# Kernel optimization log

Measured on AMD Instinct MI355X. Metric: run time of the kernel, lower is better.

## Reference

```python
import jax, jax.numpy as jnp
import numpy as np

N = 20000; E = 320000; G = 64; IN = 64; HID = 128; H = 8; HD = H * HID  # 1024


def setup_inputs() -> dict:
    key = jax.random.key(0)
    ks = jax.random.split(key, 32)
    inp = {}
    inp['x'] = jax.random.normal(ks[0], (N, IN), jnp.float32)
    inp['edge_index'] = jax.random.randint(ks[1], (2, E), 0, N, dtype=jnp.int64)
    inp['batch'] = jnp.sort(jax.random.randint(ks[2], (N,), 0, G, dtype=jnp.int64))
    dims_in = [IN, HD, HD]
    k = 3
    for i in range(3):
        d_in = dims_in[i]
        inp[f'gat_W{i}'] = jax.random.normal(ks[k], (d_in, HD), jnp.float32) * (1.0 / np.sqrt(d_in)); k += 1
        inp[f'gat_b{i}'] = jnp.zeros((HD,), jnp.float32)
        inp[f'att_src{i}'] = jax.random.normal(ks[k], (H, HID), jnp.float32) * 0.1; k += 1
        inp[f'att_dst{i}'] = jax.random.normal(ks[k], (H, HID), jnp.float32) * 0.1; k += 1
    for i in range(2):
        inp[f'boot_W{i}'] = jax.random.normal(ks[k], (HD, HD), jnp.float32) * (1.0 / np.sqrt(HD)); k += 1
        inp[f'boot_b{i}'] = jnp.zeros((HD,), jnp.float32)
    inp['clf_W1'] = jax.random.normal(ks[k], (HD, HID), jnp.float32) * (1.0 / np.sqrt(HD)); k += 1
    inp['clf_b1'] = jnp.zeros((HID,), jnp.float32)
    inp['clf_W2'] = jax.random.normal(ks[k], (HID, 2), jnp.float32) * (1.0 / np.sqrt(HID)); k += 1
    inp['clf_b2'] = jnp.zeros((2,), jnp.float32)
    return inp


def _gat_layer(x, W, b, a_src, a_dst, src, dst):
    # PyG GATConv (concat=True, self-loops already appended, eval mode => no dropout)
    h = (x @ W).reshape(N, H, HID)                      # [N,H,D]
    s = jnp.einsum('nhd,hd->nh', h, a_src)              # [N,H]
    t = jnp.einsum('nhd,hd->nh', h, a_dst)              # [N,H]
    e = jax.nn.leaky_relu(s[src] + t[dst], 0.2)         # [Etot,H]
    m = jax.ops.segment_max(e, dst, num_segments=N)     # segment softmax over incoming edges
    m = jnp.where(jnp.isfinite(m), m, 0.0)
    ex = jnp.exp(e - m[dst])
    denom = jax.ops.segment_sum(ex, dst, num_segments=N)
    alpha = ex / jnp.maximum(denom[dst], 1e-16)         # [Etot,H]
    out = jax.ops.segment_sum(alpha[:, :, None] * h[src], dst, num_segments=N)  # [N,H,D]
    return out.reshape(N, HD) + b


def reference(x, edge_index, batch,
              gat_W0, gat_b0, att_src0, att_dst0,
              gat_W1, gat_b1, att_src1, att_dst1,
              gat_W2, gat_b2, att_src2, att_dst2,
              boot_W0, boot_b0, boot_W1, boot_b1,
              clf_W1, clf_b1, clf_W2, clf_b2):
    loop = jnp.arange(N, dtype=edge_index.dtype)
    src = jnp.concatenate([edge_index[0], loop])
    dst = jnp.concatenate([edge_index[1], loop])
    gat = [(gat_W0, gat_b0, att_src0, att_dst0),
           (gat_W1, gat_b1, att_src1, att_dst1),
           (gat_W2, gat_b2, att_src2, att_dst2)]
    boot = [(boot_W0, boot_b0), (boot_W1, boot_b1)]
    h = x
    for i in range(3):
        W, b, a_s, a_d = gat[i]
        h = jax.nn.elu(_gat_layer(h, W, b, a_s, a_d, src, dst))
        if i < 2:
            noise = jax.random.normal(jax.random.key(100 + i), h.shape, h.dtype) * 0.1
            bW, bb = boot[i]
            h = (h + noise) @ bW + bb
    # global mean pool over graphs
    sums = jax.ops.segment_sum(h, batch, num_segments=G)        # [G,HD]
    cnts = jax.ops.segment_sum(jnp.ones((N,), h.dtype), batch, num_segments=G)
    g = sums / jnp.maximum(cnts, 1.0)[:, None]
    z = jax.nn.relu(g @ clf_W1 + clf_b1)                        # dropout = identity (eval)
    return z @ clf_W2 + clf_b2
```

## Files before the change

### kernel.cpp

```cpp
#include <hip/hip_runtime.h>
#include <stdint.h>

#define N_NODES 20000
#define N_EDGES 320000
#define E_TOT   (N_EDGES + N_NODES)
#define NGRAPH  64
#define DIN     64
#define DHID    128
#define NHEAD   8
#define HDIM    1024

typedef unsigned int u32;
typedef unsigned short u16;
typedef __bf16 bfx8 __attribute__((ext_vector_type(8)));
typedef float f32x4 __attribute__((ext_vector_type(4)));
typedef float f32x2 __attribute__((ext_vector_type(2)));

__device__ __forceinline__ u16 f2bf(float f){
  u32 u = __float_as_uint(f);
  u32 r = (u + 0x7FFFu + ((u >> 16) & 1u)) >> 16;
  return (u16)r;
}
__device__ __forceinline__ float bf2f(u16 v){
  return __uint_as_float(((u32)v) << 16);
}

typedef __attribute__((address_space(3))) u32 lds_u32_t;
typedef const __attribute__((address_space(1))) u32 glb_u32_t;
__device__ __forceinline__ void g2l16(const void* g, void* l){
  __builtin_amdgcn_global_load_lds((glb_u32_t*)(uintptr_t)g,
                                   (lds_u32_t*)(uintptr_t)l, 16, 0, 0);
}

__device__ __forceinline__ u32 rotl32(u32 x, int r){ return (x<<r) | (x>>(32-r)); }

__device__ __forceinline__ void threefry2x32(u32 k0, u32 k1, u32 x0, u32 x1,
                                             u32& y0, u32& y1){
  u32 k2 = k0 ^ k1 ^ 0x1BD11BDAu;
  x0 += k0; x1 += k1;
#define TFR(r) { x0 += x1; x1 = rotl32(x1, (r)); x1 ^= x0; }
  TFR(13) TFR(15) TFR(26) TFR(6)
  x0 += k1; x1 += k2 + 1u;
  TFR(17) TFR(29) TFR(16) TFR(24)
  x0 += k2; x1 += k0 + 2u;
  TFR(13) TFR(15) TFR(26) TFR(6)
  x0 += k0; x1 += k1 + 3u;
  TFR(17) TFR(29) TFR(16) TFR(24)
  x0 += k1; x1 += k2 + 4u;
  TFR(13) TFR(15) TFR(26) TFR(6)
  x0 += k2; x1 += k0 + 5u;
#undef TFR
  y0 = x0; y1 = x1;
}

__device__ __forceinline__ float erfinv_fast(float x){
  float t = fmaf(-x, x, 1.0f);
  float w = -__logf(t);
  float p;
  if (w < 5.0f){
    w -= 2.5f;
    p = 2.81022636e-08f;
    p = fmaf(p, w, 3.43273939e-07f);
    p = fmaf(p, w, -3.5233877e-06f);
    p = fmaf(p, w, -4.39150654e-06f);
    p = fmaf(p, w, 0.00021858087f);
    p = fmaf(p, w, -0.00125372503f);
    p = fmaf(p, w, -0.00417768164f);
    p = fmaf(p, w, 0.246640727f);
    p = fmaf(p, w, 1.50140941f);
  } else {
    w = sqrtf(w) - 3.0f;
    p = -0.000200214257f;
    p = fmaf(p, w, 0.000100950558f);
    p = fmaf(p, w, 0.00134934322f);
    p = fmaf(p, w, -0.00367342844f);
    p = fmaf(p, w, 0.00573950773f);
    p = fmaf(p, w, -0.0076224613f);
    p = fmaf(p, w, 0.00943887047f);
    p = fmaf(p, w, 1.00167406f);
    p = fmaf(p, w, 2.83297682f);
  }
  return p * x;
}

__device__ __forceinline__ float jax_normal(u32 seed, u32 i){
  u32 y0, y1;
  threefry2x32(0u, seed, 0u, i, y0, y1);
  u32 bits = y0 ^ y1;
  float f = __uint_as_float((bits >> 9) | 0x3f800000u) - 1.0f;
  float xx = fmaxf(-0.99999994f, fmaf(f, 2.0f, -0.99999994f));
  return 1.41421356f * erfinv_fast(xx);
}

__global__ __launch_bounds__(256) void convert3_kernel(const float* __restrict__ x,
    const float* __restrict__ W0, const float* __restrict__ W1,
    u16* __restrict__ xbf, u16* __restrict__ O0, u16* __restrict__ O1){
  const int z = blockIdx.y;
  const float* S = (z==0) ? W0 : (z==1) ? W1 : x;
  u16* D = (z==0) ? O0 : (z==1) ? O1 : xbf;
  const int total = (z==2) ? N_NODES*DIN : HDIM*HDIM;
  int i = (blockIdx.x*256 + threadIdx.x)*4;
  if (i < total){
    float4 v = *(const float4*)(S + i);
    D[i+0] = f2bf(v.x); D[i+1] = f2bf(v.y);
    D[i+2] = f2bf(v.z); D[i+3] = f2bf(v.w);
  }
}

__global__ __launch_bounds__(256) void transpose_all_kernel(
    const float* __restrict__ W0, const float* __restrict__ W1,
    const float* __restrict__ W2, const float* __restrict__ W3,
    const float* __restrict__ W4,
    u16* __restrict__ T0, u16* __restrict__ T1, u16* __restrict__ T2,
    u16* __restrict__ T3, u16* __restrict__ T4){
  const int z = blockIdx.z;
  const float* W = (z==0)?W0:(z==1)?W1:(z==2)?W2:(z==3)?W3:W4;
  u16* T = (z==0)?T0:(z==1)?T1:(z==2)?T2:(z==3)?T3:T4;
  const int K = (z==0)?DIN:HDIM;
  const int bk = blockIdx.y*32;
  if (bk >= K) return;
  __shared__ float t[32][33];
  int bn = blockIdx.x*32;
  int lx = threadIdx.x & 31, ly = threadIdx.x >> 5;
#pragma unroll
  for (int r = 0; r < 32; r += 8)
    t[ly+r][lx] = W[(size_t)(bk+ly+r)*HDIM + bn + lx];
  __syncthreads();
#pragma unroll
  for (int r = 0; r < 32; r += 8)
    T[(size_t)(bn+ly+r)*K + bk + lx] = f2bf(t[lx][ly+r]);
}

__global__ __launch_bounds__(256) void bias_pair_kernel(
    const float* __restrict__ bb0, const u16* __restrict__ gwt0,
    const float* __restrict__ bb1, const u16* __restrict__ gwt1,
    float* __restrict__ out0, float* __restrict__ out1){
  const float* bb = blockIdx.y ? bb1 : bb0;
  const u16* gwt  = blockIdx.y ? gwt1 : gwt0;
  float* out      = blockIdx.y ? out1 : out0;
  const int wv = threadIdx.x >> 6, lane = threadIdx.x & 63;
  const int n = blockIdx.x*4 + wv;
  const u16* row = gwt + (size_t)n*HDIM + lane*16;
  const float* bp = bb + lane*16;
  float acc = 0.f;
#pragma unroll
  for (int k = 0; k < 16; ++k) acc = fmaf(bp[k], bf2f(row[k]), acc);
  for (int off = 32; off > 0; off >>= 1) acc += __shfl_down(acc, off);
  if (lane == 0) out[n] = acc;
}

__global__ __launch_bounds__(256) void count_all_kernel(const int* __restrict__ ei,
    const int* __restrict__ batch, int* __restrict__ cnt, int* __restrict__ gcnt){
  int i = blockIdx.x*256 + threadIdx.x;
  if (i < N_EDGES) atomicAdd(&cnt[ei[N_EDGES + i]], 1);
  else if (i < N_EDGES + N_NODES) atomicAdd(&gcnt[batch[i - N_EDGES]], 1);
}

__global__ __launch_bounds__(1024) void scan_rowptr_kernel(const int* __restrict__ cnt,
    int* __restrict__ rowptr, int* __restrict__ cursor){
  __shared__ int wsum[16];
  __shared__ int carry_s;
  const int tid = threadIdx.x, lane = tid & 63, wv = tid >> 6;
  if (tid == 0){ carry_s = 0; rowptr[0] = 0; }
  __syncthreads();
  for (int base = 0; base < N_NODES; base += 1024){
    int i = base + tid;
    int v = (i < N_NODES) ? cnt[i] + 1 : 0;
    int s = v;
#pragma unroll
    for (int off = 1; off < 64; off <<= 1){
      int t = __shfl_up(s, off);
      if (lane >= off) s += t;
    }
    if (lane == 63) wsum[wv] = s;
    __syncthreads();
    if (wv == 0 && lane < 16){
      int ws = wsum[lane];
#pragma unroll
      for (int off = 1; off < 16; off <<= 1){
        int t = __shfl_up(ws, off);
        if (lane >= off) ws += t;
      }
      wsum[lane] = ws;
    }
    __syncthreads();
    int incl = s + ((wv > 0) ? wsum[wv-1] : 0) + carry_s;
    if (i < N_NODES){ rowptr[i+1] = incl; cursor[i] = incl - v; }
    __syncthreads();
    if (tid == 1023) carry_s = incl;
    __syncthreads();
  }
}

__global__ __launch_bounds__(256) void fill_self_kernel(int* __restrict__ cursor,
    int* __restrict__ colidx){
  int n = blockIdx.x*256 + threadIdx.x;
  if (n < N_NODES){ int p = atomicAdd(&cursor[n], 1); colidx[p] = n; }
}

__global__ __launch_bounds__(256) void fill_edges_kernel(const int* __restrict__ ei,
    int* __restrict__ cursor, int* __restrict__ colidx){
  int e = blockIdx.x*256 + threadIdx.x;
  if (e < N_EDGES){
    int s = ei[e], d = ei[N_EDGES + e];
    int p = atomicAdd(&cursor[d], 1);
    colidx[p] = s;
  }
}

__global__ void scan_gcnt_kernel(const int* __restrict__ gcnt, int* __restrict__ goff){
  if (threadIdx.x == 0){
    int s = 0;
    for (int g = 0; g < NGRAPH; ++g){ goff[g] = s; s += gcnt[g]; }
    goff[NGRAPH] = s;
  }
}

__device__ __forceinline__ void gemm_tile(const u16* __restrict__ A,
    const u16* __restrict__ BT, const float* __restrict__ bias,
    u16* __restrict__ Cb, int M, int K, int bm, int bn,
    u16* As, u16* Bs){
  const int tid = threadIdx.x;
  const int lane = tid & 63, w = tid >> 6;
  const int wm = (w & 1)*64, wn = (w >> 1)*64;

  const int cid0 = tid, cid1 = 256 + tid;
  const int r0 = cid0 & 127, kc0 = cid0 >> 7;
  const int r1 = cid1 & 127, kc1 = cid1 >> 7;
  int ar0 = bm + r0; if (ar0 >= M) ar0 = M - 1;
  int ar1 = bm + r1; if (ar1 >= M) ar1 = M - 1;
  const u16* ag0 = A + (size_t)ar0*K + kc0*8;
  const u16* ag1 = A + (size_t)ar1*K + kc1*8;
  const u16* bg0 = BT + (size_t)(bn + r0)*K + kc0*8;
  const u16* bg1 = BT + (size_t)(bn + r1)*K + kc1*8;
  u16* al0 = As + cid0*8;  u16* al1 = As + cid1*8;
  u16* bl0 = Bs + cid0*8;  u16* bl1 = Bs + cid1*8;

  const int rowl = lane & 15, kg = lane >> 4;
  const bfx8* ap = (const bfx8*)(As + ((size_t)kg*128 + wm + rowl)*8);
  const bfx8* bp = (const bfx8*)(Bs + ((size_t)kg*128 + wn + rowl)*8);

  f32x4 acc[4][4] = {};
  for (int k0 = 0; k0 < K; k0 += 32){
    g2l16(ag0 + k0, al0);
    g2l16(ag1 + k0, al1);
    g2l16(bg0 + k0, bl0);
    g2l16(bg1 + k0, bl1);
    __syncthreads();
    bfx8 af[4], bfr[4];
#pragma unroll
    for (int i = 0; i < 4; ++i){ af[i] = ap[i*16]; bfr[i] = bp[i*16]; }
#pragma unroll
    for (int i = 0; i < 4; ++i)
#pragma unroll
      for (int j = 0; j < 4; ++j)
        acc[j][i] = __builtin_amdgcn_mfma_f32_16x16x32_bf16(bfr[j], af[i], acc[j][i], 0, 0, 0);
    __syncthreads();
  }

  const int quad = lane >> 4;
#pragma unroll
  for (int j = 0; j < 4; ++j){
    const int col0 = bn + wn + j*16 + quad*4;
    float4 bv = make_float4(0.f,0.f,0.f,0.f);
    if (bias) bv = *(const float4*)(bias + col0);
#pragma unroll
    for (int i = 0; i < 4; ++i){
      const int row = bm + wm + i*16 + rowl;
      if (row < M){
        const u16 p0 = f2bf(acc[j][i][0] + bv.x);
        const u16 p1 = f2bf(acc[j][i][1] + bv.y);
        const u16 p2 = f2bf(acc[j][i][2] + bv.z);
        const u16 p3 = f2bf(acc[j][i][3] + bv.w);
        uint2 pk;
        pk.x = (u32)p0 | ((u32)p1 << 16);
        pk.y = (u32)p2 | ((u32)p3 << 16);
        *(uint2*)(Cb + (size_t)row*HDIM + col0) = pk;
      }
    }
  }
}

__global__ __launch_bounds__(256) void gemm_bf16(
    const u16* __restrict__ A, const u16* __restrict__ BT,
    const float* __restrict__ bias, u16* __restrict__ Cb, int M, int K){
  __shared__ __align__(16) u16 As[4*128*8];
  __shared__ __align__(16) u16 Bs[4*128*8];
  const int kblk = blockIdx.y*8 + blockIdx.x;
  const int xc = kblk & 7, bq = (kblk >> 3) & 7, gq = kblk >> 6;
  const int bmi = gq*8 + xc;
  const int mt = (M + 127) >> 7;
  if (bmi >= mt) return;
  gemm_tile(A, BT, bias, Cb, M, K, bmi*128, bq*128, As, Bs);
}

__global__ __launch_bounds__(256) void gemm_wf_pair(
    const u16* __restrict__ A0, const u16* __restrict__ B0, u16* __restrict__ C0,
    const u16* __restrict__ A1, const u16* __restrict__ B1, u16* __restrict__ C1){
  __shared__ __align__(16) u16 As[4*128*8];
  __shared__ __align__(16) u16 Bs[4*128*8];
  const u16* A = blockIdx.z ? A1 : A0;
  const u16* B = blockIdx.z ? B1 : B0;
  u16* C = blockIdx.z ? C1 : C0;
  gemm_tile(A, B, nullptr, C, HDIM, HDIM, blockIdx.y*128, blockIdx.x*128, As, Bs);
}

__global__ __launch_bounds__(256) void st_kernel(const u16* __restrict__ h,
    const float* __restrict__ asrc, const float* __restrict__ adst,
    float* __restrict__ sbuf, float* __restrict__ tbuf){
  int gid = blockIdx.x*4 + (threadIdx.x >> 6);
  if (gid >= N_NODES*NHEAD) return;
  int lane = threadIdx.x & 63;
  int n = gid >> 3, hh = gid & 7;
  const u16* hp = h + (size_t)n*HDIM + hh*DHID;
  const float* ap = asrc + hh*DHID;
  const float* bp = adst + hh*DHID;
  ushort2 hv = *(const ushort2*)(hp + lane*2);
  float h0 = bf2f(hv.x), h1 = bf2f(hv.y);
  float a0 = ap[lane*2], a1 = ap[lane*2+1];
  float b0 = bp[lane*2], b1 = bp[lane*2+1];
  float sv = fmaf(h0, a0, h1*a1);
  float tv = fmaf(h0, b0, h1*b1);
  for (int off = 32; off > 0; off >>= 1){
    sv += __shfl_down(sv, off);
    tv += __shfl_down(tv, off);
  }
  if (lane == 0){ sbuf[gid] = sv; tbuf[gid] = tv; }
}

__global__ __launch_bounds__(256) void gat_agg_kernel(const u16* __restrict__ hlin,
    const float* __restrict__ sbuf, const float* __restrict__ tbuf,
    const int* __restrict__ rowptr, const int* __restrict__ colidx,
    const float* __restrict__ bias, float* __restrict__ outf,
    u16* __restrict__ outbf, u32 seed){
  __shared__ float esh[64*NHEAD];
  __shared__ int   srcs[64];
  __shared__ float tn[NHEAD], mh[NHEAD], dsum[NHEAD], resc[NHEAD];
  const int n = blockIdx.x;
  const int tid = threadIdx.x;
  const int ht = tid >> 5;
  if (tid < NHEAD){
    tn[tid] = tbuf[n*NHEAD + tid];
    mh[tid] = -INFINITY;
    dsum[tid] = 0.0f;
  }
  const int row0 = rowptr[n];
  const int deg = rowptr[n+1] - row0;
  const char* hl = (const char*)hlin;
  const u32 tid8 = (u32)tid*8u;
  const char* sbase = (const char*)sbuf;
  f32x2 a01 = {0.f,0.f}, a23 = {0.f,0.f};
  f32x2 b01 = {0.f,0.f}, b23 = {0.f,0.f};
  for (int c = 0; c < deg; c += 64){
    const int nc = min(64, deg - c);
    __syncthreads();
    if (tid < nc) srcs[tid] = colidx[row0 + c + tid] << 11;
    __syncthreads();
    for (int it = tid; it < nc*NHEAD; it += 256){
      int j = it >> 3, hh = it & 7;
      const float* sp = (const float*)(sbase + (srcs[j] >> 6));
      float e = sp[hh] + tn[hh];
      esh[it] = (e > 0.f) ? e : 0.2f*e;
    }
    __syncthreads();
    if (tid < 64){
      const int hh = tid & 7, slot = tid >> 3;
      float mc = -INFINITY;
      for (int j = slot; j < nc; j += 8) mc = fmaxf(mc, esh[j*NHEAD+hh]);
      mc = fmaxf(mc, __shfl_xor(mc, 8));
      mc = fmaxf(mc, __shfl_xor(mc, 16));
      mc = fmaxf(mc, __shfl_xor(mc, 32));
      const float mold = mh[hh];
      const float mnew = fmaxf(mold, mc);
      float wsum = 0.f;
      for (int j = slot; j < nc; j += 8){
        float w = __expf(esh[j*NHEAD+hh] - mnew);
        esh[j*NHEAD+hh] = w;
        wsum += w;
      }
      wsum += __shfl_xor(wsum, 8);
      wsum += __shfl_xor(wsum, 16);
      wsum += __shfl_xor(wsum, 32);
      if (slot == 0){
        float r = (mold == -INFINITY) ? 0.0f : __expf(mold - mnew);
        dsum[hh] = fmaf(dsum[hh], r, wsum);
        mh[hh] = mnew;
        resc[hh] = r;
      }
    }
    __syncthreads();
    const float r = resc[ht];
    const f32x2 r2 = {r, r};
    a01 *= r2; a23 *= r2; b01 *= r2; b23 *= r2;
    int j = 0;
    for (; j + 2 <= nc; j += 2){
      const float w0 = esh[j*NHEAD + ht];
      const float w1 = esh[(j+1)*NHEAD + ht];
      const char* rp0 = hl + (u32)__builtin_amdgcn_readfirstlane(srcs[j]);
      const char* rp1 = hl + (u32)__builtin_amdgcn_readfirstlane(srcs[j+1]);
      const uint2 h0 = *(const uint2*)(rp0 + tid8);
      const uint2 h1 = *(const uint2*)(rp1 + tid8);
      const f32x2 w02 = {w0, w0}, w12 = {w1, w1};
      f32x2 v;
      v.x = __uint_as_float(h0.x << 16); v.y = __uint_as_float(h0.x & 0xffff0000u);
      a01 = __builtin_elementwise_fma(w02, v, a01);
      v.x = __uint_as_float(h0.y << 16); v.y = __uint_as_float(h0.y & 0xffff0000u);
      a23 = __builtin_elementwise_fma(w02, v, a23);
      v.x = __uint_as_float(h1.x << 16); v.y = __uint_as_float(h1.x & 0xffff0000u);
      b01 = __builtin_elementwise_fma(w12, v, b01);
      v.x = __uint_as_float(h1.y << 16); v.y = __uint_as_float(h1.y & 0xffff0000u);
      b23 = __builtin_elementwise_fma(w12, v, b23);
    }
    if (j < nc){
      const float w0 = esh[j*NHEAD + ht];
      const char* rp0 = hl + (u32)__builtin_amdgcn_readfirstlane(srcs[j]);
      const uint2 h0 = *(const uint2*)(rp0 + tid8);
      const f32x2 w02 = {w0, w0};
      f32x2 v;
      v.x = __uint_as_float(h0.x << 16); v.y = __uint_as_float(h0.x & 0xffff0000u);
      a01 = __builtin_elementwise_fma(w02, v, a01);
      v.x = __uint_as_float(h0.y << 16); v.y = __uint_as_float(h0.y & 0xffff0000u);
      a23 = __builtin_elementwise_fma(w02, v, a23);
    }
  }
  float4 acc = make_float4(a01.x + b01.x, a01.y + b01.y,
                           a23.x + b23.x, a23.y + b23.y);
  const float inv = 1.0f / fmaxf(dsum[ht], 1e-16f);
  const float4 bv = *(const float4*)(bias + tid*4);
  float4 o;
  o.x = fmaf(acc.x, inv, bv.x);
  o.y = fmaf(acc.y, inv, bv.y);
  o.z = fmaf(acc.z, inv, bv.z);
  o.w = fmaf(acc.w, inv, bv.w);
  o.x = (o.x > 0.f) ? o.x : __expf(o.x) - 1.0f;
  o.y = (o.y > 0.f) ? o.y : __expf(o.y) - 1.0f;
  o.z = (o.z > 0.f) ? o.z : __expf(o.z) - 1.0f;
  o.w = (o.w > 0.f) ? o.w : __expf(o.w) - 1.0f;
  if (outbf){
    const u32 ib = (u32)(n*HDIM + tid*4);
    ushort4 ov;
    ov.x = f2bf(fmaf(0.1f, jax_normal(seed, ib+0u), o.x));
    ov.y = f2bf(fmaf(0.1f, jax_normal(seed, ib+1u), o.y));
    ov.z = f2bf(fmaf(0.1f, jax_normal(seed, ib+2u), o.z));
    ov.w = f2bf(fmaf(0.1f, jax_normal(seed, ib+3u), o.w));
    *(ushort4*)(outbf + (size_t)n*HDIM + tid*4) = ov;
  } else {
    *(float4*)(outf + (size_t)n*HDIM + tid*4) = o;
  }
}

__global__ __launch_bounds__(64) void pool_kernel(const float* __restrict__ h,
    const int* __restrict__ goff, const int* __restrict__ gcnt,
    float* __restrict__ gpool){
  int g = blockIdx.x;
  int cb = blockIdx.y*256 + threadIdx.x*4;
  float4 acc = make_float4(0.f,0.f,0.f,0.f);
  int n0 = goff[g], n1 = goff[g+1];
  for (int n = n0; n < n1; ++n){
    const float4 v = *(const float4*)(h + (size_t)n*HDIM + cb);
    acc.x += v.x; acc.y += v.y; acc.z += v.z; acc.w += v.w;
  }
  float invc = 1.0f / fmaxf((float)gcnt[g], 1.0f);
  acc.x *= invc; acc.y *= invc; acc.z *= invc; acc.w *= invc;
  *(float4*)(gpool + g*HDIM + cb) = acc;
}

__global__ __launch_bounds__(128) void clf_kernel(const float* __restrict__ gpool,
    const float* __restrict__ W1, const float* __restrict__ b1,
    const float* __restrict__ W2, const float* __restrict__ b2,
    float* __restrict__ out){
  __shared__ float gs[HDIM];
  __shared__ float z[DHID];
  int g = blockIdx.x, tid = threadIdx.x;
  for (int k = tid; k < HDIM; k += 128) gs[k] = gpool[g*HDIM + k];
  __syncthreads();
  float acc = b1[tid];
  for (int k = 0; k < HDIM; ++k) acc = fmaf(gs[k], W1[k*DHID + tid], acc);
  z[tid] = fmaxf(acc, 0.0f);
  __syncthreads();
  if (tid < 2){
    float o = b2[tid];
    for (int k = 0; k < DHID; ++k) o = fmaf(z[k], W2[k*2 + tid], o);
    out[g*2 + tid] = o;
  }
}

extern "C" void kernel_launch(void* const* d_in, const int* in_sizes, int n_in,
                              void* d_out, int out_size, void* d_ws, size_t ws_size,
                              hipStream_t stream){
  const float* x      = (const float*)d_in[0];
  const int*   ei     = (const int*)d_in[1];
  const int*   batch  = (const int*)d_in[2];
  const float* gatW[3]  = {(const float*)d_in[3],  (const float*)d_in[7],  (const float*)d_in[11]};
  const float* gatB[3]  = {(const float*)d_in[4],  (const float*)d_in[8],  (const float*)d_in[12]};
  const float* asrc[3]  = {(const float*)d_in[5],  (const float*)d_in[9],  (const float*)d_in[13]};
  const float* adst[3]  = {(const float*)d_in[6],  (const float*)d_in[10], (const float*)d_in[14]};
  const float* bootW[2] = {(const float*)d_in[15], (const float*)d_in[17]};
  const float* bootB[2] = {(const float*)d_in[16], (const float*)d_in[18]};
  const float* clfW1 = (const float*)d_in[19];
  const float* clfb1 = (const float*)d_in[20];
  const float* clfW2 = (const float*)d_in[21];
  const float* clfb2 = (const float*)d_in[22];
  float* outp = (float*)d_out;

  float* fws  = (float*)d_ws;
  float* hB   = fws;
  float* sbuf = hB + (size_t)N_NODES*HDIM;
  float* tbuf = sbuf + (size_t)N_NODES*NHEAD;
  float* gpool= tbuf + (size_t)N_NODES*NHEAD;
  float* fbias0 = gpool + NGRAPH*HDIM;
  float* fbias1 = fbias0 + HDIM;
  u16* xbf    = (u16*)(fbias1 + HDIM);
  u16* hAbf   = xbf + (size_t)N_NODES*DIN;
  u16* hBbf   = hAbf + (size_t)N_NODES*HDIM;
  u16* wt[3];
  wt[0] = hBbf + (size_t)N_NODES*HDIM;
  wt[1] = wt[0] + (size_t)HDIM*DIN;
  wt[2] = wt[1] + (size_t)HDIM*HDIM;
  u16* wtd0   = wt[2] + (size_t)HDIM*HDIM;
  u16* wtd1   = wtd0 + (size_t)HDIM*HDIM;
  u16* wnt0   = wtd1 + (size_t)HDIM*HDIM;
  u16* wnt1   = wnt0 + (size_t)HDIM*HDIM;
  u16* wf0    = wnt1 + (size_t)HDIM*HDIM;
  u16* wf1    = wf0 + (size_t)HDIM*HDIM;
  int* rowptr = (int*)(wf1 + (size_t)HDIM*HDIM);
  int* cursor = rowptr + (N_NODES+1);
  int* colidx = cursor + N_NODES;
  int* gcnt   = colidx + E_TOT;
  int* cnt    = gcnt + NGRAPH;
  int* goff   = cnt + N_NODES;

  hipMemsetAsync(gcnt, 0, (NGRAPH + N_NODES)*sizeof(int), stream);

  const int nb_n = (N_NODES + 255)/256;
  const int nb_e = (N_EDGES + 255)/256;
  count_all_kernel<<<(N_EDGES + N_NODES + 255)/256, 256, 0, stream>>>(ei, batch, cnt, gcnt);
  scan_rowptr_kernel<<<1, 1024, 0, stream>>>(cnt, rowptr, cursor);
  fill_self_kernel<<<nb_n, 256, 0, stream>>>(cursor, colidx);
  fill_edges_kernel<<<nb_e, 256, 0, stream>>>(ei, cursor, colidx);
  scan_gcnt_kernel<<<1, 64, 0, stream>>>(gcnt, goff);

  convert3_kernel<<<dim3((N_NODES*DIN/4 + 255)/256, 3), 256, 0, stream>>>(
      x, bootW[0], bootW[1], xbf, wnt0, wnt1);
  transpose_all_kernel<<<dim3(HDIM/32, HDIM/32, 5), 256, 0, stream>>>(
      gatW[0], gatW[1], gatW[2], bootW[0], bootW[1],
      wt[0], wt[1], wt[2], wtd0, wtd1);

  gemm_wf_pair<<<dim3(8, 8, 2), 256, 0, stream>>>(wt[1], wnt0, wf0, wt[2], wnt1, wf1);
  bias_pair_kernel<<<dim3(HDIM/4, 2), 256, 0, stream>>>(
      bootB[0], wt[1], bootB[1], wt[2], fbias0, fbias1);

  const int mt = (N_NODES + 127)/128;
  dim3 gemmGrid(8, (mt + 7)/8*8);
  const int stGrid = (N_NODES*NHEAD)/4;

  gemm_bf16<<<gemmGrid, 256, 0, stream>>>(xbf, wt[0], nullptr, hAbf, N_NODES, DIN);
  st_kernel<<<stGrid, 256, 0, stream>>>(hAbf, asrc[0], adst[0], sbuf, tbuf);
  gat_agg_kernel<<<N_NODES, 256, 0, stream>>>(hAbf, sbuf, tbuf, rowptr, colidx,
                                              gatB[0], nullptr, hBbf, 100u);
  gemm_bf16<<<gemmGrid, 256, 0, stream>>>(hBbf, wf0, fbias0, hAbf, N_NODES, HDIM);
  st_kernel<<<stGrid, 256, 0, stream>>>(hAbf, asrc[1], adst[1], sbuf, tbuf);
  gat_agg_kernel<<<N_NODES, 256, 0, stream>>>(hAbf, sbuf, tbuf, rowptr, colidx,
                                              gatB[1], nullptr, hBbf, 101u);
  gemm_bf16<<<gemmGrid, 256, 0, stream>>>(hBbf, wf1, fbias1, hAbf, N_NODES, HDIM);
  st_kernel<<<stGrid, 256, 0, stream>>>(hAbf, asrc[2], adst[2], sbuf, tbuf);
  gat_agg_kernel<<<N_NODES, 256, 0, stream>>>(hAbf, sbuf, tbuf, rowptr, colidx,
                                              gatB[2], hB, nullptr, 0u);

  pool_kernel<<<dim3(NGRAPH, HDIM/256), 64, 0, stream>>>(hB, goff, gcnt, gpool);
  clf_kernel<<<NGRAPH, 128, 0, stream>>>(gpool, clfW1, clfb1, clfW2, clfb2, outp);
}
```

Before: 1.017 ms.

## Fuse attention score dot-products into GEMM epilogue and merge prep kernels

Computes the per-node, per-head source and destination attention scores inside the GEMM epilogue. Each block reduces its 128-column head slice using lane shuffles and a shared-memory exchange between wave pairs, which removes the separate st_kernel pass that re-read the full 20000x1024 bf16 activation three times. It also merges the small setup kernels (convert plus count, the two scans, wf GEMM plus bias) to cut launch count. The cost is extra epilogue work and an added block barrier in the GEMM.

```diff
diff --git a/kernel.cpp b/kernel.cpp
--- a/kernel.cpp
+++ b/kernel.cpp
@@ -92,18 +92,26 @@
   return 1.41421356f * erfinv_fast(xx);
 }
 
-__global__ __launch_bounds__(256) void convert3_kernel(const float* __restrict__ x,
+__global__ __launch_bounds__(256) void prep_misc_kernel(const float* __restrict__ x,
     const float* __restrict__ W0, const float* __restrict__ W1,
-    u16* __restrict__ xbf, u16* __restrict__ O0, u16* __restrict__ O1){
+    u16* __restrict__ xbf, u16* __restrict__ O0, u16* __restrict__ O1,
+    const int* __restrict__ ei, const int* __restrict__ batch,
+    int* __restrict__ cnt, int* __restrict__ gcnt){
   const int z = blockIdx.y;
-  const float* S = (z==0) ? W0 : (z==1) ? W1 : x;
-  u16* D = (z==0) ? O0 : (z==1) ? O1 : xbf;
-  const int total = (z==2) ? N_NODES*DIN : HDIM*HDIM;
-  int i = (blockIdx.x*256 + threadIdx.x)*4;
-  if (i < total){
-    float4 v = *(const float4*)(S + i);
-    D[i+0] = f2bf(v.x); D[i+1] = f2bf(v.y);
-    D[i+2] = f2bf(v.z); D[i+3] = f2bf(v.w);
+  if (z < 3){
+    const float* S = (z==0) ? W0 : (z==1) ? W1 : x;
+    u16* D = (z==0) ? O0 : (z==1) ? O1 : xbf;
+    const int total = (z==2) ? N_NODES*DIN : HDIM*HDIM;
+    int i = (blockIdx.x*256 + threadIdx.x)*4;
+    if (i < total){
+      float4 v = *(const float4*)(S + i);
+      D[i+0] = f2bf(v.x); D[i+1] = f2bf(v.y);
+      D[i+2] = f2bf(v.z); D[i+3] = f2bf(v.w);
+    }
+  } else {
+    int i = blockIdx.x*256 + threadIdx.x;
+    if (i < N_EDGES) atomicAdd(&cnt[ei[N_EDGES + i]], 1);
+    else if (i < E_TOT) atomicAdd(&gcnt[batch[i - N_EDGES]], 1);
   }
 }
 
@@ -131,33 +139,17 @@
     T[(size_t)(bn+ly+r)*K + bk + lx] = f2bf(t[lx][ly+r]);
 }
 
-__global__ __launch_bounds__(256) void bias_pair_kernel(
-    const float* __restrict__ bb0, const u16* __restrict__ gwt0,
-    const float* __restrict__ bb1, const u16* __restrict__ gwt1,
-    float* __restrict__ out0, float* __restrict__ out1){
-  const float* bb = blockIdx.y ? bb1 : bb0;
-  const u16* gwt  = blockIdx.y ? gwt1 : gwt0;
-  float* out      = blockIdx.y ? out1 : out0;
-  const int wv = threadIdx.x >> 6, lane = threadIdx.x & 63;
-  const int n = blockIdx.x*4 + wv;
-  const u16* row = gwt + (size_t)n*HDIM + lane*16;
-  const float* bp = bb + lane*16;
-  float acc = 0.f;
-#pragma unroll
-  for (int k = 0; k < 16; ++k) acc = fmaf(bp[k], bf2f(row[k]), acc);
-  for (int off = 32; off > 0; off >>= 1) acc += __shfl_down(acc, off);
-  if (lane == 0) out[n] = acc;
-}
-
-__global__ __launch_bounds__(256) void count_all_kernel(const int* __restrict__ ei,
-    const int* __restrict__ batch, int* __restrict__ cnt, int* __restrict__ gcnt){
-  int i = blockIdx.x*256 + threadIdx.x;
-  if (i < N_EDGES) atomicAdd(&cnt[ei[N_EDGES + i]], 1);
-  else if (i < N_EDGES + N_NODES) atomicAdd(&gcnt[batch[i - N_EDGES]], 1);
-}
-
-__global__ __launch_bounds__(1024) void scan_rowptr_kernel(const int* __restrict__ cnt,
-    int* __restrict__ rowptr, int* __restrict__ cursor){
+__global__ __launch_bounds__(1024) void scan_pair_kernel(const int* __restrict__ cnt,
+    int* __restrict__ rowptr, int* __restrict__ cursor,
+    const int* __restrict__ gcnt, int* __restrict__ goff){
+  if (blockIdx.x == 1){
+    if (threadIdx.x == 0){
+      int s = 0;
+      for (int g = 0; g < NGRAPH; ++g){ goff[g] = s; s += gcnt[g]; }
+      goff[NGRAPH] = s;
+    }
+    return;
+  }
   __shared__ int wsum[16];
   __shared__ int carry_s;
   const int tid = threadIdx.x, lane = tid & 63, wv = tid >> 6;
@@ -208,18 +200,12 @@
   }
 }
 
-__global__ void scan_gcnt_kernel(const int* __restrict__ gcnt, int* __restrict__ goff){
-  if (threadIdx.x == 0){
-    int s = 0;
-    for (int g = 0; g < NGRAPH; ++g){ goff[g] = s; s += gcnt[g]; }
-    goff[NGRAPH] = s;
-  }
-}
-
 __device__ __forceinline__ void gemm_tile(const u16* __restrict__ A,
     const u16* __restrict__ BT, const float* __restrict__ bias,
     u16* __restrict__ Cb, int M, int K, int bm, int bn,
-    u16* As, u16* Bs){
+    u16* As, u16* Bs,
+    const float* __restrict__ asrc, const float* __restrict__ adst,
+    float* __restrict__ sbuf, float* __restrict__ tbuf){
   const int tid = threadIdx.x;
   const int lane = tid & 63, w = tid >> 6;
   const int wm = (w & 1)*64, wn = (w >> 1)*64;
@@ -259,31 +245,75 @@
   }
 
   const int quad = lane >> 4;
+  const bool dost = (sbuf != nullptr);
+  const int head = bn >> 7;
+  float sl[4] = {0.f,0.f,0.f,0.f}, tl[4] = {0.f,0.f,0.f,0.f};
 #pragma unroll
   for (int j = 0; j < 4; ++j){
     const int col0 = bn + wn + j*16 + quad*4;
     float4 bv = make_float4(0.f,0.f,0.f,0.f);
     if (bias) bv = *(const float4*)(bias + col0);
+    float4 av = make_float4(0.f,0.f,0.f,0.f), dv = av;
+    if (dost){
+      const int d0 = col0 - bn;
+      av = *(const float4*)(asrc + head*DHID + d0);
+      dv = *(const float4*)(adst + head*DHID + d0);
+    }
 #pragma unroll
     for (int i = 0; i < 4; ++i){
       const int row = bm + wm + i*16 + rowl;
+      const u16 p0 = f2bf(acc[j][i][0] + bv.x);
+      const u16 p1 = f2bf(acc[j][i][1] + bv.y);
+      const u16 p2 = f2bf(acc[j][i][2] + bv.z);
+      const u16 p3 = f2bf(acc[j][i][3] + bv.w);
       if (row < M){
-        const u16 p0 = f2bf(acc[j][i][0] + bv.x);
-        const u16 p1 = f2bf(acc[j][i][1] + bv.y);
-        const u16 p2 = f2bf(acc[j][i][2] + bv.z);
-        const u16 p3 = f2bf(acc[j][i][3] + bv.w);
         uint2 pk;
         pk.x = (u32)p0 | ((u32)p1 << 16);
         pk.y = (u32)p2 | ((u32)p3 << 16);
         *(uint2*)(Cb + (size_t)row*HDIM + col0) = pk;
       }
+      if (dost){
+        const float c0 = bf2f(p0), c1 = bf2f(p1), c2 = bf2f(p2), c3 = bf2f(p3);
+        sl[i] = fmaf(c0, av.x, fmaf(c1, av.y, fmaf(c2, av.z, fmaf(c3, av.w, sl[i]))));
+        tl[i] = fmaf(c0, dv.x, fmaf(c1, dv.y, fmaf(c2, dv.z, fmaf(c3, dv.w, tl[i]))));
+      }
+    }
+  }
+  if (dost){
+#pragma unroll
+    for (int i = 0; i < 4; ++i){
+      sl[i] += __shfl_xor(sl[i], 16); sl[i] += __shfl_xor(sl[i], 32);
+      tl[i] += __shfl_xor(tl[i], 16); tl[i] += __shfl_xor(tl[i], 32);
+    }
+    float* sred = (float*)As;
+    float* tred = sred + 128;
+    if ((w >> 1) == 0 && quad == 0){
+#pragma unroll
+      for (int i = 0; i < 4; ++i){
+        const int rl = wm + i*16 + rowl;
+        sred[rl] = sl[i]; tred[rl] = tl[i];
+      }
+    }
+    __syncthreads();
+    if ((w >> 1) == 1 && quad == 0){
+#pragma unroll
+      for (int i = 0; i < 4; ++i){
+        const int rl = wm + i*16 + rowl;
+        const int row = bm + rl;
+        if (row < M){
+          sbuf[row*NHEAD + head] = sred[rl] + sl[i];
+          tbuf[row*NHEAD + head] = tred[rl] + tl[i];
+        }
+      }
     }
   }
 }
 
 __global__ __launch_bounds__(256) void gemm_bf16(
     const u16* __restrict__ A, const u16* __restrict__ BT,
-    const float* __restrict__ bias, u16* __restrict__ Cb, int M, int K){
+    const float* __restrict__ bias, u16* __restrict__ Cb, int M, int K,
+    const float* __restrict__ asrc, const float* __restrict__ adst,
+    float* __restrict__ sbuf, float* __restrict__ tbuf){
   __shared__ __align__(16) u16 As[4*128*8];
   __shared__ __align__(16) u16 Bs[4*128*8];
   const int kblk = blockIdx.y*8 + blockIdx.x;
@@ -291,41 +321,39 @@
   const int bmi = gq*8 + xc;
   const int mt = (M + 127) >> 7;
   if (bmi >= mt) return;
-  gemm_tile(A, BT, bias, Cb, M, K, bmi*128, bq*128, As, Bs);
-}
-
-__global__ __launch_bounds__(256) void gemm_wf_pair(
+  gemm_tile(A, BT, bias, Cb, M, K, bmi*128, bq*128, As, Bs,
+            asrc, adst, sbuf, tbuf);
+}
+
+__global__ __launch_bounds__(256) void wf_bias_kernel(
     const u16* __restrict__ A0, const u16* __restrict__ B0, u16* __restrict__ C0,
-    const u16* __restrict__ A1, const u16* __restrict__ B1, u16* __restrict__ C1){
+    const u16* __restrict__ A1, const u16* __restrict__ B1, u16* __restrict__ C1,
+    const float* __restrict__ bb0, const u16* __restrict__ gwt0,
+    const float* __restrict__ bb1, const u16* __restrict__ gwt1,
+    float* __restrict__ fb0, float* __restrict__ fb1){
   __shared__ __align__(16) u16 As[4*128*8];
   __shared__ __align__(16) u16 Bs[4*128*8];
-  const u16* A = blockIdx.z ? A1 : A0;
-  const u16* B = blockIdx.z ? B1 : B0;
-  u16* C = blockIdx.z ? C1 : C0;
-  gemm_tile(A, B, nullptr, C, HDIM, HDIM, blockIdx.y*128, blockIdx.x*128, As, Bs);
-}
-
-__global__ __launch_bounds__(256) void st_kernel(const u16* __restrict__ h,
-    const float* __restrict__ asrc, const float* __restrict__ adst,
-    float* __restrict__ sbuf, float* __restrict__ tbuf){
-  int gid = blockIdx.x*4 + (threadIdx.x >> 6);
-  if (gid >= N_NODES*NHEAD) return;
-  int lane = threadIdx.x & 63;
-  int n = gid >> 3, hh = gid & 7;
-  const u16* hp = h + (size_t)n*HDIM + hh*DHID;
-  const float* ap = asrc + hh*DHID;
-  const float* bp = adst + hh*DHID;
-  ushort2 hv = *(const ushort2*)(hp + lane*2);
-  float h0 = bf2f(hv.x), h1 = bf2f(hv.y);
-  float a0 = ap[lane*2], a1 = ap[lane*2+1];
-  float b0 = bp[lane*2], b1 = bp[lane*2+1];
-  float sv = fmaf(h0, a0, h1*a1);
-  float tv = fmaf(h0, b0, h1*b1);
-  for (int off = 32; off > 0; off >>= 1){
-    sv += __shfl_down(sv, off);
-    tv += __shfl_down(tv, off);
-  }
-  if (lane == 0){ sbuf[gid] = sv; tbuf[gid] = tv; }
+  if (blockIdx.z < 2){
+    const u16* A = blockIdx.z ? A1 : A0;
+    const u16* B = blockIdx.z ? B1 : B0;
+    u16* C = blockIdx.z ? C1 : C0;
+    gemm_tile(A, B, nullptr, C, HDIM, HDIM, blockIdx.y*128, blockIdx.x*128,
+              As, Bs, nullptr, nullptr, nullptr, nullptr);
+  } else {
+    const int kb = blockIdx.y*8 + blockIdx.x;
+    const int wv = threadIdx.x >> 6, lane = threadIdx.x & 63;
+    for (int idx = kb*4 + wv; idx < 2*HDIM; idx += 256){
+      const int set = idx >> 10, n = idx & (HDIM-1);
+      const float* bb = set ? bb1 : bb0;
+      const u16* row = (set ? gwt1 : gwt0) + (size_t)n*HDIM + lane*16;
+      const float* bp = bb + lane*16;
+      float acc = 0.f;
+#pragma unroll
+      for (int k = 0; k < 16; ++k) acc = fmaf(bp[k], bf2f(row[k]), acc);
+      for (int off = 32; off > 0; off >>= 1) acc += __shfl_down(acc, off);
+      if (lane == 0) (set ? fb1 : fb0)[n] = acc;
+    }
+  }
 }
 
 __global__ __launch_bounds__(256) void gat_agg_kernel(const u16* __restrict__ hlin,
@@ -534,36 +562,33 @@
 
   const int nb_n = (N_NODES + 255)/256;
   const int nb_e = (N_EDGES + 255)/256;
-  count_all_kernel<<<(N_EDGES + N_NODES + 255)/256, 256, 0, stream>>>(ei, batch, cnt, gcnt);
-  scan_rowptr_kernel<<<1, 1024, 0, stream>>>(cnt, rowptr, cursor);
-  fill_self_kernel<<<nb_n, 256, 0, stream>>>(cursor, colidx);
-  fill_edges_kernel<<<nb_e, 256, 0, stream>>>(ei, cursor, colidx);
-  scan_gcnt_kernel<<<1, 64, 0, stream>>>(gcnt, goff);
-
-  convert3_kernel<<<dim3((N_NODES*DIN/4 + 255)/256, 3), 256, 0, stream>>>(
-      x, bootW[0], bootW[1], xbf, wnt0, wnt1);
+
+  prep_misc_kernel<<<dim3((E_TOT + 255)/256, 4), 256, 0, stream>>>(
+      x, bootW[0], bootW[1], xbf, wnt0, wnt1, ei, batch, cnt, gcnt);
   transpose_all_kernel<<<dim3(HDIM/32, HDIM/32, 5), 256, 0, stream>>>(
       gatW[0], gatW[1], gatW[2], bootW[0], bootW[1],
       wt[0], wt[1], wt[2], wtd0, wtd1);
-
-  gemm_wf_pair<<<dim3(8, 8, 2), 256, 0, stream>>>(wt[1], wnt0, wf0, wt[2], wnt1, wf1);
-  bias_pair_kernel<<<dim3(HDIM/4, 2), 256, 0, stream>>>(
+  scan_pair_kernel<<<2, 1024, 0, stream>>>(cnt, rowptr, cursor, gcnt, goff);
+  fill_self_kernel<<<nb_n, 256, 0, stream>>>(cursor, colidx);
+  fill_edges_kernel<<<nb_e, 256, 0, stream>>>(ei, cursor, colidx);
+
+  wf_bias_kernel<<<dim3(8, 8, 3), 256, 0, stream>>>(
+      wt[1], wnt0, wf0, wt[2], wnt1, wf1,
       bootB[0], wt[1], bootB[1], wt[2], fbias0, fbias1);
 
   const int mt = (N_NODES + 127)/128;
   dim3 gemmGrid(8, (mt + 7)/8*8);
-  const int stGrid = (N_NODES*NHEAD)/4;
-
-  gemm_bf16<<<gemmGrid, 256, 0, stream>>>(xbf, wt[0], nullptr, hAbf, N_NODES, DIN);
-  st_kernel<<<stGrid, 256, 0, stream>>>(hAbf, asrc[0], adst[0], sbuf, tbuf);
+
+  gemm_bf16<<<gemmGrid, 256, 0, stream>>>(xbf, wt[0], nullptr, hAbf, N_NODES, DIN,
+                                          asrc[0], adst[0], sbuf, tbuf);
   gat_agg_kernel<<<N_NODES, 256, 0, stream>>>(hAbf, sbuf, tbuf, rowptr, colidx,
                                               gatB[0], nullptr, hBbf, 100u);
-  gemm_bf16<<<gemmGrid, 256, 0, stream>>>(hBbf, wf0, fbias0, hAbf, N_NODES, HDIM);
-  st_kernel<<<stGrid, 256, 0, stream>>>(hAbf, asrc[1], adst[1], sbuf, tbuf);
+  gemm_bf16<<<gemmGrid, 256, 0, stream>>>(hBbf, wf0, fbias0, hAbf, N_NODES, HDIM,
+                                          asrc[1], adst[1], sbuf, tbuf);
   gat_agg_kernel<<<N_NODES, 256, 0, stream>>>(hAbf, sbuf, tbuf, rowptr, colidx,
                                               gatB[1], nullptr, hBbf, 101u);
-  gemm_bf16<<<gemmGrid, 256, 0, stream>>>(hBbf, wf1, fbias1, hAbf, N_NODES, HDIM);
-  st_kernel<<<stGrid, 256, 0, stream>>>(hAbf, asrc[2], adst[2], sbuf, tbuf);
+  gemm_bf16<<<gemmGrid, 256, 0, stream>>>(hBbf, wf1, fbias1, hAbf, N_NODES, HDIM,
+                                          asrc[2], adst[2], sbuf, tbuf);
   gat_agg_kernel<<<N_NODES, 256, 0, stream>>>(hAbf, sbuf, tbuf, rowptr, colidx,
                                               gatB[2], hB, nullptr, 0u);
 
```

Measured after the change: 952.8 us. -6.3%, faster.
